# Optimization experiments

Hardware: AMD Instinct MI355X
Metric: run time of the kernel (lower is better)

Reference implementation:

```python
import jax, jax.numpy as jnp
import numpy as np

B, H, W, C = 32, 56, 56, 256
WS = 7            # window size (hard-coded 49=7*7 in original topk modules)
NH = 8            # num heads
HD = C // NH      # head dim = 32
KCH = HD // 2     # channel top-k = 16
KSPT = 28         # spatial top-k
N = WS * WS       # 49 tokens per window
SCALE = HD ** -0.5
MLP_H = 4 * C

def _rel_index(ws):
    coords = np.stack(np.meshgrid(np.arange(ws), np.arange(ws), indexing='ij')).reshape(2, -1)
    rc = (coords[:, :, None] - coords[:, None, :]).transpose(1, 2, 0).astype(np.int64)
    rc[:, :, 0] += ws - 1
    rc[:, :, 1] += ws - 1
    rc[:, :, 0] *= 2 * ws - 1
    return jnp.asarray(rc.sum(-1))  # (N, N)

REL_IDX = _rel_index(WS)

def setup_inputs():
    key = jax.random.key(0)
    ks = jax.random.split(key, 10)
    p = lambda k, shp: jax.random.normal(k, shp, jnp.float32) * 0.02
    return dict(
        x=jax.random.normal(ks[0], (B, H * W, C), jnp.float32),
        norm1_g=jnp.ones((C,), jnp.float32), norm1_b=jnp.zeros((C,), jnp.float32),
        wq=p(ks[1], (C, C)), bq=jnp.zeros((C,), jnp.float32),
        wk=p(ks[2], (C // 2, C // 2)), bk=jnp.zeros((C // 2,), jnp.float32),
        wv=p(ks[3], (C, C)), bv=jnp.zeros((C,), jnp.float32),
        wproj=p(ks[4], (C, C)), bproj=jnp.zeros((C,), jnp.float32),
        wch=p(ks[5], (2 * HD, HD)), bch=jnp.zeros((HD,), jnp.float32),
        rpb_table=p(ks[6], ((2 * WS - 1) ** 2, NH)),
        norm2_g=jnp.ones((C,), jnp.float32), norm2_b=jnp.zeros((C,), jnp.float32),
        w1=p(ks[7], (C, MLP_H)), b1=jnp.zeros((MLP_H,), jnp.float32),
        w2=p(ks[8], (MLP_H, C)), b2=jnp.zeros((C,), jnp.float32),
    )

def _ln(x, g, b):
    mu = x.mean(-1, keepdims=True)
    var = x.var(-1, keepdims=True)
    return (x - mu) / jnp.sqrt(var + 1e-5) * g + b

def reference(x, norm1_g, norm1_b, wq, bq, wk, bk, wv, bv, wproj, bproj,
              wch, bch, rpb_table, norm2_g, norm2_b, w1, b1, w2, b2):
    shortcut = x
    xn = _ln(x, norm1_g, norm1_b).reshape(B, H, W, C)
    # window partition -> (Bw, N, C)
    xw = xn.reshape(B, H // WS, WS, W // WS, WS, C).transpose(0, 1, 3, 2, 4, 5).reshape(-1, N, C)
    Bw = xw.shape[0]
    q = xw @ wq + bq                                                    # (Bw, N, C)
    qh = q.reshape(Bw, N, NH, HD).transpose(0, 2, 1, 3).reshape(Bw * NH, N, HD)
    # ---- channel top-k (ChannelTopk) ----
    feat = jnp.concatenate([qh.mean(1), qh.max(1)], axis=-1)            # (Bn, 2*HD)
    score = jax.nn.softmax(jax.nn.gelu(feat @ wch + bch, approximate=False), axis=1)
    _, cidx = jax.lax.top_k(score, KCH)
    cidx = jnp.sort(cidx, axis=-1)                                      # sorted channel indices
    qcha = jnp.take_along_axis(qh, cidx[:, None, :], axis=2)            # (Bn, N, KCH)
    qcha1 = qcha.reshape(Bw, NH, N, KCH).transpose(0, 2, 1, 3).reshape(Bw, N, C // 2)
    k = qcha1 @ wk + bk                                                 # (Bw, N, C/2)
    # ---- relative position bias ----
    rpb = rpb_table[REL_IDX.reshape(-1)].reshape(N, N, NH).transpose(2, 0, 1)  # (NH, N, N)
    # ---- spatial top-k (SptialTopk) ----
    _, sidx = jax.lax.top_k(qh.mean(-1), KSPT)
    sidx = jnp.sort(sidx, axis=-1)                                      # (Bn, KSPT)
    qal = jnp.take_along_axis(qcha, sidx[:, :, None], axis=1)           # (Bn, KSPT, KCH)
    vsel = jnp.take_along_axis(qh, sidx[:, :, None], axis=1)            # (Bn, KSPT, HD)
    sidx_h = sidx.reshape(Bw, NH, KSPT)
    yal = jnp.take_along_axis(
        jnp.broadcast_to(rpb[None], (Bw, NH, N, N)),
        jnp.broadcast_to(sidx_h[:, :, None, :], (Bw, NH, N, KSPT)), axis=-1)  # (Bw, NH, N, KSPT)
    # ---- attention ----
    v = vsel.reshape(Bw, NH, KSPT, HD).transpose(0, 2, 1, 3).reshape(Bw, KSPT, C)
    v = (v @ wv + bv).reshape(Bw, KSPT, NH, HD).transpose(0, 2, 1, 3)   # (Bw, NH, KSPT, HD)
    qspt = (qal * SCALE).reshape(Bw, NH, KSPT, KCH)
    kh = k.reshape(Bw, N, NH, KCH).transpose(0, 2, 1, 3)                # (Bw, NH, N, KCH)
    attn = jnp.einsum('bnqc,bnkc->bnqk', kh, qspt) + yal                # (Bw, NH, N, KSPT)
    gate = jax.nn.sigmoid(attn.mean(-1))                                # (Bw, NH, N)
    attn = jax.nn.softmax(attn, axis=-1)
    o = jnp.einsum('bnqk,bnkd->bnqd', attn, v) * gate[..., None]        # (Bw, NH, N, HD)
    o = o.transpose(0, 2, 1, 3).reshape(Bw, N, C)
    o = o @ wproj + bproj
    # window reverse -> (B, L, C)
    xr = o.reshape(B, H // WS, W // WS, WS, WS, C).transpose(0, 1, 3, 2, 4, 5).reshape(B, H * W, C)
    x = shortcut + xr
    h = jax.nn.gelu(_ln(x, norm2_g, norm2_b) @ w1 + b1, approximate=False)
    return x + h @ w2 + b2
```

## Files before the change

kernel.cpp:

```cpp
#include <hip/hip_runtime.h>
#include <hip/hip_bf16.h>
#include <cmath>

#define CC 256
#define WSZ 7
#define WWD_ 56
#define NHD 8
#define HDIM 32
#define KCHN 16
#define KSP 28
#define NTOK 49
#define NWIN 2048
#define NBH 16384
#define LL 3136
#define MTOK 100352
#define MLPH 1024
#define SCALE_Q 0.17677669529663689f

typedef float floatx4 __attribute__((ext_vector_type(4)));
typedef __bf16 bf16x8_t __attribute__((ext_vector_type(8)));

__device__ __forceinline__ float gelu_f(float x) {
    return 0.5f * x * (1.0f + erff(x * 0.7071067811865475f));
}

__global__ __launch_bounds__(64) void ln_stats_k(const float* __restrict__ x,
                                                 float* __restrict__ mu,
                                                 float* __restrict__ rs) {
    int row = blockIdx.x;
    int lane = threadIdx.x;
    float4 v = reinterpret_cast<const float4*>(x + (size_t)row * CC)[lane];
    float s = v.x + v.y + v.z + v.w;
    float s2 = v.x * v.x + v.y * v.y + v.z * v.z + v.w * v.w;
#pragma unroll
    for (int off = 32; off > 0; off >>= 1) {
        s += __shfl_down(s, off);
        s2 += __shfl_down(s2, off);
    }
    if (lane == 0) {
        float m = s * (1.0f / CC);
        float var = s2 * (1.0f / CC) - m * m;
        mu[row] = m;
        rs[row] = rsqrtf(var + 1e-5f);
    }
}

struct GP {
    const float* W;
    const float* bias;
    float* C;
    int N, K;
    const float* x;
    const float* mu;
    const float* rs;
    const float* g;
    const float* be;
};

__global__ __launch_bounds__(256) void gemm_q_k(GP p) {
    constexpr int BM = 64, BN = 64, BK = 16;
    __shared__ float As[BK][BM + 4];
    __shared__ float Bs[BK][BN + 4];
    const int bm = blockIdx.x * BM;
    const int bn = blockIdx.y * BN;
    const int tid = threadIdx.x;
    const int tx = tid & 15;
    const int ty = tid >> 4;
    const int rowA = tid >> 2;
    const int ka4 = (tid & 3) << 2;
    const int rowB = tid >> 4;
    const int nb4 = (tid & 15) << 2;
    float acc[4][4] = {};

    const int r = bm + rowA;
    int bwi = r / NTOK, n = r - bwi * NTOK;
    int b = bwi >> 6, rem = bwi & 63;
    int hw = rem >> 3, ww = rem & 7;
    int i0 = n / WSZ, j0 = n - i0 * WSZ;
    size_t grow = (size_t)b * LL + (size_t)(hw * WSZ + i0) * WWD_ + (ww * WSZ + j0);

    for (int k0 = 0; k0 < p.K; k0 += BK) {
        {
            const int kk = k0 + ka4;
            float m = p.mu[grow], rsg = p.rs[grow];
            float4 xv = *reinterpret_cast<const float4*>(p.x + grow * CC + kk);
            float4 gv = *reinterpret_cast<const float4*>(p.g + kk);
            float4 bv = *reinterpret_cast<const float4*>(p.be + kk);
            As[ka4 + 0][rowA] = (xv.x - m) * rsg * gv.x + bv.x;
            As[ka4 + 1][rowA] = (xv.y - m) * rsg * gv.y + bv.y;
            As[ka4 + 2][rowA] = (xv.z - m) * rsg * gv.z + bv.z;
            As[ka4 + 3][rowA] = (xv.w - m) * rsg * gv.w + bv.w;
        }
        {
            float4 bv = *reinterpret_cast<const float4*>(p.W + (size_t)(k0 + rowB) * p.N + bn + nb4);
            Bs[rowB][nb4 + 0] = bv.x;
            Bs[rowB][nb4 + 1] = bv.y;
            Bs[rowB][nb4 + 2] = bv.z;
            Bs[rowB][nb4 + 3] = bv.w;
        }
        __syncthreads();
#pragma unroll
        for (int kk = 0; kk < BK; ++kk) {
            float a[4], bb[4];
#pragma unroll
            for (int u = 0; u < 4; ++u) {
                a[u] = As[kk][ty * 4 + u];
                bb[u] = Bs[kk][tx * 4 + u];
            }
#pragma unroll
            for (int i = 0; i < 4; ++i)
#pragma unroll
                for (int j = 0; j < 4; ++j) acc[i][j] = fmaf(a[i], bb[j], acc[i][j]);
        }
        __syncthreads();
    }
#pragma unroll
    for (int i = 0; i < 4; ++i) {
        const int rr = bm + ty * 4 + i;
#pragma unroll
        for (int j = 0; j < 4; ++j) {
            const int nn = bn + tx * 4 + j;
            p.C[(size_t)rr * p.N + nn] = acc[i][j] + p.bias[nn];
        }
    }
}

struct MG {
    const __hip_bfloat16* A;
    const __hip_bfloat16* B;
    const float* bias;
    int N, K;
    float* Cf;
    __hip_bfloat16* Cb;
    const float* resid;
    int row0;
};

template <int EPI>
__global__ __launch_bounds__(256) void mgemm_k(MG p) {
    __shared__ __align__(16) __hip_bfloat16 As[128 * 32];
    __shared__ __align__(16) __hip_bfloat16 Bs[128 * 32];
    const int bm = blockIdx.x * 128;
    const int bn = blockIdx.y * 128;
    const int t = threadIdx.x;
    const int lane = t & 63;
    const int w = t >> 6;
    const int wm = (w & 1) * 64;
    const int wn = (w >> 1) * 64;
    const int fr = lane & 15;
    const int fk = (lane >> 4) * 8;

    const int m0 = t >> 2, m1 = (t + 256) >> 2;
    const int kc = (t & 3) * 8;
    const __hip_bfloat16* a0 = p.A + (size_t)(bm + m0) * p.K + kc;
    const __hip_bfloat16* a1 = p.A + (size_t)(bm + m1) * p.K + kc;
    const __hip_bfloat16* b0 = p.B + (size_t)(bn + m0) * p.K + kc;
    const __hip_bfloat16* b1 = p.B + (size_t)(bn + m1) * p.K + kc;

    floatx4 acc[4][4] = {};

    for (int k0 = 0; k0 < p.K; k0 += 32) {
        *(uint4*)&As[m0 * 32 + kc] = *(const uint4*)(a0 + k0);
        *(uint4*)&As[m1 * 32 + kc] = *(const uint4*)(a1 + k0);
        *(uint4*)&Bs[m0 * 32 + kc] = *(const uint4*)(b0 + k0);
        *(uint4*)&Bs[m1 * 32 + kc] = *(const uint4*)(b1 + k0);
        __syncthreads();
        bf16x8_t af[4], bf[4];
#pragma unroll
        for (int i = 0; i < 4; ++i)
            af[i] = *(const bf16x8_t*)&As[(wm + i * 16 + fr) * 32 + fk];
#pragma unroll
        for (int j = 0; j < 4; ++j)
            bf[j] = *(const bf16x8_t*)&Bs[(wn + j * 16 + fr) * 32 + fk];
#pragma unroll
        for (int i = 0; i < 4; ++i)
#pragma unroll
            for (int j = 0; j < 4; ++j)
                acc[i][j] = __builtin_amdgcn_mfma_f32_16x16x32_bf16(af[i], bf[j], acc[i][j], 0, 0, 0);
        __syncthreads();
    }

    float bj[4];
#pragma unroll
    for (int j = 0; j < 4; ++j) bj[j] = p.bias[bn + wn + j * 16 + fr];
#pragma unroll
    for (int i = 0; i < 4; ++i) {
#pragma unroll
        for (int r = 0; r < 4; ++r) {
            const int m = bm + wm + i * 16 + (lane >> 4) * 4 + r;
#pragma unroll
            for (int j = 0; j < 4; ++j) {
                const int n = bn + wn + j * 16 + fr;
                float v = acc[i][j][r] + bj[j];
                if constexpr (EPI == 0) {
                    p.Cb[(size_t)m * p.N + n] = __float2bfloat16(v);
                } else if constexpr (EPI == 1) {
                    int bwi = m / NTOK, nn = m - bwi * NTOK;
                    int b = bwi >> 6, rem = bwi & 63;
                    int hw = rem >> 3, wwp = rem & 7;
                    int ii = nn / WSZ, jj = nn - ii * WSZ;
                    size_t oidx = ((size_t)b * LL + (size_t)(hw * WSZ + ii) * WWD_ + (wwp * WSZ + jj)) * CC + n;
                    p.Cf[oidx] = v + p.resid[oidx];
                } else if constexpr (EPI == 2) {
                    p.Cb[(size_t)m * p.N + n] = __float2bfloat16(gelu_f(v));
                } else {
                    size_t gr = (size_t)(m + p.row0);
                    p.Cf[gr * p.N + n] = v + p.resid[gr * p.N + n];
                }
            }
        }
    }
}

__global__ __launch_bounds__(256) void wt_k(const float* __restrict__ W,
                                            __hip_bfloat16* __restrict__ Wt, int K, int N) {
    int g = blockIdx.x * 256 + threadIdx.x;
    if (g >= K * N) return;
    int n = g / K, kk = g - n * K;
    Wt[g] = __float2bfloat16(W[(size_t)kk * N + n]);
}

__global__ __launch_bounds__(64) void topk_k(const float* __restrict__ q,
                                             const float* __restrict__ wch,
                                             const float* __restrict__ bch,
                                             short* __restrict__ cidx,
                                             short* __restrict__ sidx) {
    int bnh = blockIdx.x;
    int bwi = bnh >> 3, h = bnh & 7;
    int lane = threadIdx.x;
    __shared__ float tile[NTOK][HDIM + 1];
    __shared__ float feat[2 * HDIM];
    __shared__ float score[HDIM];
    __shared__ float rowm[NTOK];
    const float* qbase = q + ((size_t)bwi * NTOK) * CC + h * HDIM;
    for (int idx = lane; idx < NTOK * HDIM; idx += 64) {
        int n = idx >> 5, d = idx & 31;
        tile[n][d] = qbase[(size_t)n * CC + d];
    }
    __syncthreads();
    if (lane < HDIM) {
        float s = 0.f, mx = -INFINITY;
        for (int n = 0; n < NTOK; ++n) {
            float v = tile[n][lane];
            s += v;
            mx = fmaxf(mx, v);
        }
        feat[lane] = s * (1.0f / NTOK);
        feat[HDIM + lane] = mx;
    }
    if (lane < NTOK) {
        float s = 0.f;
        for (int d = 0; d < HDIM; ++d) s += tile[lane][d];
        rowm[lane] = s;
    }
    __syncthreads();
    if (lane < HDIM) {
        float s = bch[lane];
        for (int j = 0; j < 2 * HDIM; ++j) s += feat[j] * wch[j * HDIM + lane];
        score[lane] = gelu_f(s);
    }
    __syncthreads();
    {
        bool sel = false;
        if (lane < HDIM) {
            float sv = score[lane];
            int rank = 0;
            for (int j = 0; j < HDIM; ++j) {
                float oj = score[j];
                rank += (oj > sv) || (oj == sv && j < lane);
            }
            sel = rank < KCHN;
        }
        unsigned long long m = __ballot(sel);
        if (sel) {
            int pos = __popcll(m & ((1ull << lane) - 1ull));
            cidx[(size_t)bnh * KCHN + pos] = (short)lane;
        }
    }
    {
        bool sel = false;
        if (lane < NTOK) {
            float sv = rowm[lane];
            int rank = 0;
            for (int j = 0; j < NTOK; ++j) {
                float oj = rowm[j];
                rank += (oj > sv) || (oj == sv && j < lane);
            }
            sel = rank < KSP;
        }
        unsigned long long m = __ballot(sel);
        if (sel) {
            int pos = __popcll(m & ((1ull << lane) - 1ull));
            sidx[(size_t)bnh * KSP + pos] = (short)lane;
        }
    }
}

__global__ __launch_bounds__(256) void gather_ch_k(const float* __restrict__ q,
                                                   const short* __restrict__ cidx,
                                                   __hip_bfloat16* __restrict__ ak) {
    int g = blockIdx.x * 256 + threadIdx.x;
    int r = g >> 7, kk = g & 127;
    int bwi = r / NTOK;
    int hp = kk >> 4, c = kk & 15;
    int ci = cidx[((size_t)(bwi * NHD + hp)) * KCHN + c];
    ak[g] = __float2bfloat16(q[(size_t)r * CC + hp * HDIM + ci]);
}

__global__ __launch_bounds__(256) void gather_sp_k(const float* __restrict__ q,
                                                   const short* __restrict__ sidx,
                                                   __hip_bfloat16* __restrict__ av) {
    int g = blockIdx.x * 256 + threadIdx.x;
    int rr = g >> 8, c = g & 255;
    int bwi = rr / KSP, s = rr - bwi * KSP;
    int tok = sidx[((size_t)(bwi * NHD + (c >> 5))) * KSP + s];
    av[g] = __float2bfloat16(q[((size_t)(bwi * NTOK + tok)) * CC + c]);
}

__global__ __launch_bounds__(64) void attn_k(const float* __restrict__ q,
                                             const __hip_bfloat16* __restrict__ kb,
                                             const __hip_bfloat16* __restrict__ vb,
                                             const short* __restrict__ cidx,
                                             const short* __restrict__ sidx,
                                             const float* __restrict__ rpb,
                                             __hip_bfloat16* __restrict__ ob) {
    int bnh = blockIdx.x;
    int bwi = bnh >> 3, h = bnh & 7;
    int lane = threadIdx.x;
    __shared__ float kh_s[NTOK][KCHN + 1];
    __shared__ float qs_s[KSP][KCHN];
    __shared__ float v_s[KSP][HDIM];
    __shared__ int sidx_s[KSP];
    __shared__ int cidx_s[KCHN];
    if (lane < KSP) sidx_s[lane] = sidx[(size_t)bnh * KSP + lane];
    if (lane < KCHN) cidx_s[lane] = cidx[(size_t)bnh * KCHN + lane];
    for (int idx = lane; idx < NTOK * KCHN; idx += 64) {
        int n = idx >> 4, c = idx & 15;
        kh_s[n][c] = __bfloat162float(kb[((size_t)bwi * NTOK + n) * (NHD * KCHN) + h * KCHN + c]);
    }
    for (int idx = lane; idx < KSP * HDIM; idx += 64) {
        int s = idx >> 5, d = idx & 31;
        v_s[s][d] = __bfloat162float(vb[((size_t)bwi * KSP + s) * CC + h * HDIM + d]);
    }
    __syncthreads();
    for (int idx = lane; idx < KSP * KCHN; idx += 64) {
        int s = idx >> 4, c = idx & 15;
        qs_s[s][c] = q[((size_t)bwi * NTOK + sidx_s[s]) * CC + h * HDIM + cidx_s[c]] * SCALE_Q;
    }
    __syncthreads();
    if (lane < NTOK) {
        int i1 = lane / WSZ, j1 = lane - i1 * WSZ;
        float a[KSP];
        float msum = 0.f;
#pragma unroll
        for (int s = 0; s < KSP; ++s) {
            float dot = 0.f;
#pragma unroll
            for (int c = 0; c < KCHN; ++c) dot += kh_s[lane][c] * qs_s[s][c];
            int m = sidx_s[s];
            int i2 = m / WSZ, j2 = m - i2 * WSZ;
            float bias = rpb[(size_t)((i1 - i2 + 6) * 13 + (j1 - j2 + 6)) * NHD + h];
            a[s] = dot + bias;
            msum += a[s];
        }
        float gate = 1.0f / (1.0f + expf(-msum * (1.0f / KSP)));
        float mx = -INFINITY;
#pragma unroll
        for (int s = 0; s < KSP; ++s) mx = fmaxf(mx, a[s]);
        float sum = 0.f;
#pragma unroll
        for (int s = 0; s < KSP; ++s) {
            a[s] = expf(a[s] - mx);
            sum += a[s];
        }
        float inv = gate / sum;
        __hip_bfloat16* orow = ob + ((size_t)bwi * NTOK + lane) * CC + h * HDIM;
#pragma unroll
        for (int d = 0; d < HDIM; ++d) {
            float od = 0.f;
#pragma unroll
            for (int s = 0; s < KSP; ++s) od += a[s] * v_s[s][d];
            orow[d] = __float2bfloat16(od * inv);
        }
    }
}

__global__ __launch_bounds__(64) void ln2_k(const float* __restrict__ x2,
                                            const float* __restrict__ g,
                                            const float* __restrict__ b,
                                            __hip_bfloat16* __restrict__ a2) {
    int row = blockIdx.x;
    int lane = threadIdx.x;
    float4 v = reinterpret_cast<const float4*>(x2 + (size_t)row * CC)[lane];
    float s = v.x + v.y + v.z + v.w;
    float s2 = v.x * v.x + v.y * v.y + v.z * v.z + v.w * v.w;
#pragma unroll
    for (int off = 1; off < 64; off <<= 1) {
        s += __shfl_xor(s, off);
        s2 += __shfl_xor(s2, off);
    }
    float m = s * (1.0f / CC);
    float rsg = rsqrtf(s2 * (1.0f / CC) - m * m + 1e-5f);
    float4 gv = reinterpret_cast<const float4*>(g)[lane];
    float4 bv = reinterpret_cast<const float4*>(b)[lane];
    __hip_bfloat16* orow = a2 + (size_t)row * CC + lane * 4;
    orow[0] = __float2bfloat16((v.x - m) * rsg * gv.x + bv.x);
    orow[1] = __float2bfloat16((v.y - m) * rsg * gv.y + bv.y);
    orow[2] = __float2bfloat16((v.z - m) * rsg * gv.z + bv.z);
    orow[3] = __float2bfloat16((v.w - m) * rsg * gv.w + bv.w);
}

extern "C" void kernel_launch(void* const* d_in, const int* in_sizes, int n_in,
                              void* d_out, int out_size, void* d_ws, size_t ws_size,
                              hipStream_t stream) {
    const float* x   = (const float*)d_in[0];
    const float* n1g = (const float*)d_in[1];
    const float* n1b = (const float*)d_in[2];
    const float* wq  = (const float*)d_in[3];
    const float* bq  = (const float*)d_in[4];
    const float* wk  = (const float*)d_in[5];
    const float* bk  = (const float*)d_in[6];
    const float* wv  = (const float*)d_in[7];
    const float* bv  = (const float*)d_in[8];
    const float* wpj = (const float*)d_in[9];
    const float* bpj = (const float*)d_in[10];
    const float* wch = (const float*)d_in[11];
    const float* bch = (const float*)d_in[12];
    const float* rpb = (const float*)d_in[13];
    const float* n2g = (const float*)d_in[14];
    const float* n2b = (const float*)d_in[15];
    const float* w1  = (const float*)d_in[16];
    const float* b1  = (const float*)d_in[17];
    const float* w2  = (const float*)d_in[18];
    const float* b2  = (const float*)d_in[19];
    float* out = (float*)d_out;

    char* wsb = (char*)d_ws;
    float* qb            = (float*)wsb;
    __hip_bfloat16* g1   = (__hip_bfloat16*)(wsb + 102760448);
    __hip_bfloat16* g2   = (__hip_bfloat16*)(wsb + 128450560);
    __hip_bfloat16* ob   = g1;
    __hip_bfloat16* kb   = (__hip_bfloat16*)(wsb + 157810688);
    __hip_bfloat16* vb   = (__hip_bfloat16*)(wsb + 183500800);
    float* mu1           = (float*)(wsb + 212860928);
    float* rs1           = mu1 + MTOK;
    short* cidx          = (short*)(wsb + 213663744);
    short* sidx          = (short*)(wsb + 214188032);
    __hip_bfloat16* wkt  = (__hip_bfloat16*)(wsb + 215105536);
    __hip_bfloat16* wvt  = (__hip_bfloat16*)(wsb + 215138304);
    __hip_bfloat16* wpt  = (__hip_bfloat16*)(wsb + 215269376);
    __hip_bfloat16* w1t  = (__hip_bfloat16*)(wsb + 215400448);
    __hip_bfloat16* w2t  = (__hip_bfloat16*)(wsb + 215924736);
    __hip_bfloat16* a2   = (__hip_bfloat16*)qb;
    __hip_bfloat16* hb   = (__hip_bfloat16*)(wsb + 51380224);
    if (ws_size < 216449024ULL) return;

    wt_k<<<(128 * 128 + 255) / 256, 256, 0, stream>>>(wk, wkt, 128, 128);
    wt_k<<<(256 * 256 + 255) / 256, 256, 0, stream>>>(wv, wvt, 256, 256);
    wt_k<<<(256 * 256 + 255) / 256, 256, 0, stream>>>(wpj, wpt, 256, 256);
    wt_k<<<(256 * 1024 + 255) / 256, 256, 0, stream>>>(w1, w1t, 256, 1024);
    wt_k<<<(1024 * 256 + 255) / 256, 256, 0, stream>>>(w2, w2t, 1024, 256);

    ln_stats_k<<<MTOK, 64, 0, stream>>>(x, mu1, rs1);

    GP p{};
    p.W = wq; p.bias = bq; p.C = qb; p.N = CC; p.K = CC;
    p.x = x; p.mu = mu1; p.rs = rs1; p.g = n1g; p.be = n1b;
    gemm_q_k<<<dim3(MTOK / 64, CC / 64), 256, 0, stream>>>(p);

    topk_k<<<NBH, 64, 0, stream>>>(qb, wch, bch, cidx, sidx);

    gather_ch_k<<<MTOK * 128 / 256, 256, 0, stream>>>(qb, cidx, g1);
    MG m{};
    m.A = g1; m.B = wkt; m.bias = bk; m.N = 128; m.K = 128; m.Cb = kb;
    mgemm_k<0><<<dim3(MTOK / 128, 1), 256, 0, stream>>>(m);

    gather_sp_k<<<NWIN * KSP * 256 / 256, 256, 0, stream>>>(qb, sidx, g2);
    m = MG{};
    m.A = g2; m.B = wvt; m.bias = bv; m.N = CC; m.K = CC; m.Cb = vb;
    mgemm_k<0><<<dim3(NWIN * KSP / 128, 2), 256, 0, stream>>>(m);

    attn_k<<<NBH, 64, 0, stream>>>(qb, kb, vb, cidx, sidx, rpb, ob);

    m = MG{};
    m.A = ob; m.B = wpt; m.bias = bpj; m.N = CC; m.K = CC; m.Cf = out; m.resid = x;
    mgemm_k<1><<<dim3(MTOK / 128, 2), 256, 0, stream>>>(m);

    ln2_k<<<MTOK, 64, 0, stream>>>(out, n2g, n2b, a2);

    const int CHUNK = MTOK / 4;
    for (int c = 0; c < 4; ++c) {
        int start = c * CHUNK;
        m = MG{};
        m.A = a2 + (size_t)start * CC; m.B = w1t; m.bias = b1;
        m.N = MLPH; m.K = CC; m.Cb = hb;
        mgemm_k<2><<<dim3(CHUNK / 128, MLPH / 128), 256, 0, stream>>>(m);

        m = MG{};
        m.A = hb; m.B = w2t; m.bias = b2; m.N = CC; m.K = MLPH;
        m.Cf = out; m.resid = out; m.row0 = start;
        mgemm_k<3><<<dim3(CHUNK / 128, CC / 128), 256, 0, stream>>>(m);
    }
}
```

Before: 1.147 ms.

## Widen Q GEMM tile to full N and load tiles via direct global-to-LDS DMA

After: 1.141 ms. Within noise of the previous version (-0.6%).

```diff
diff --git a/kernel.cpp b/kernel.cpp
--- a/kernel.cpp
+++ b/kernel.cpp
@@ -24,6 +24,11 @@
     return 0.5f * x * (1.0f + erff(x * 0.7071067811865475f));
 }
 
+__device__ __forceinline__ void lds_dma16(const void* g, void* l) {
+    __builtin_amdgcn_global_load_lds((__attribute__((address_space(1))) void*)(void*)g,
+                                     (__attribute__((address_space(3))) void*)l, 16, 0, 0);
+}
+
 __global__ __launch_bounds__(64) void ln_stats_k(const float* __restrict__ x,
                                                  float* __restrict__ mu,
                                                  float* __restrict__ rs) {
@@ -58,70 +63,70 @@
 };
 
 __global__ __launch_bounds__(256) void gemm_q_k(GP p) {
-    constexpr int BM = 64, BN = 64, BK = 16;
-    __shared__ float As[BK][BM + 4];
-    __shared__ float Bs[BK][BN + 4];
-    const int bm = blockIdx.x * BM;
-    const int bn = blockIdx.y * BN;
-    const int tid = threadIdx.x;
-    const int tx = tid & 15;
-    const int ty = tid >> 4;
-    const int rowA = tid >> 2;
-    const int ka4 = (tid & 3) << 2;
-    const int rowB = tid >> 4;
-    const int nb4 = (tid & 15) << 2;
-    float acc[4][4] = {};
-
-    const int r = bm + rowA;
+    __shared__ __align__(16) float As[16][68];
+    __shared__ __align__(16) float Bs[16][256];
+    const int bm = blockIdx.x * 64;
+    const int t = threadIdx.x;
+    const int tx = t & 31;
+    const int ty = t >> 5;
+    const int w = t >> 6;
+
+    const int ar = t >> 2;
+    const int ak = (t & 3) * 4;
+
+    const int r = bm + ar;
     int bwi = r / NTOK, n = r - bwi * NTOK;
     int b = bwi >> 6, rem = bwi & 63;
     int hw = rem >> 3, ww = rem & 7;
     int i0 = n / WSZ, j0 = n - i0 * WSZ;
     size_t grow = (size_t)b * LL + (size_t)(hw * WSZ + i0) * WWD_ + (ww * WSZ + j0);
-
-    for (int k0 = 0; k0 < p.K; k0 += BK) {
+    const float m = p.mu[grow], rsg = p.rs[grow];
+    const float* xrow = p.x + grow * CC;
+
+    float acc[8][8] = {};
+
+    for (int k0 = 0; k0 < CC; k0 += 16) {
         {
-            const int kk = k0 + ka4;
-            float m = p.mu[grow], rsg = p.rs[grow];
-            float4 xv = *reinterpret_cast<const float4*>(p.x + grow * CC + kk);
+            const int kk = k0 + ak;
+            float4 xv = *reinterpret_cast<const float4*>(xrow + kk);
             float4 gv = *reinterpret_cast<const float4*>(p.g + kk);
             float4 bv = *reinterpret_cast<const float4*>(p.be + kk);
-            As[ka4 + 0][rowA] = (xv.x - m) * rsg * gv.x + bv.x;
-            As[ka4 + 1][rowA] = (xv.y - m) * rsg * gv.y + bv.y;
-            As[ka4 + 2][rowA] = (xv.z - m) * rsg * gv.z + bv.z;
-            As[ka4 + 3][rowA] = (xv.w - m) * rsg * gv.w + bv.w;
-        }
-        {
-            float4 bv = *reinterpret_cast<const float4*>(p.W + (size_t)(k0 + rowB) * p.N + bn + nb4);
-            Bs[rowB][nb4 + 0] = bv.x;
-            Bs[rowB][nb4 + 1] = bv.y;
-            Bs[rowB][nb4 + 2] = bv.z;
-            Bs[rowB][nb4 + 3] = bv.w;
+            As[ak + 0][ar] = (xv.x - m) * rsg * gv.x + bv.x;
+            As[ak + 1][ar] = (xv.y - m) * rsg * gv.y + bv.y;
+            As[ak + 2][ar] = (xv.z - m) * rsg * gv.z + bv.z;
+            As[ak + 3][ar] = (xv.w - m) * rsg * gv.w + bv.w;
+        }
+#pragma unroll
+        for (int j = 0; j < 4; ++j) {
+            const int c = j * 256 + t;
+            const float* gp = p.W + (size_t)(k0 + (c >> 6)) * CC + (c & 63) * 4;
+            lds_dma16(gp, (char*)&Bs[0][0] + j * 4096 + w * 1024);
         }
         __syncthreads();
 #pragma unroll
-        for (int kk = 0; kk < BK; ++kk) {
-            float a[4], bb[4];
-#pragma unroll
-            for (int u = 0; u < 4; ++u) {
-                a[u] = As[kk][ty * 4 + u];
-                bb[u] = Bs[kk][tx * 4 + u];
-            }
-#pragma unroll
-            for (int i = 0; i < 4; ++i)
-#pragma unroll
-                for (int j = 0; j < 4; ++j) acc[i][j] = fmaf(a[i], bb[j], acc[i][j]);
+        for (int kk = 0; kk < 16; ++kk) {
+            float a[8], bb[8];
+            *(float4*)&a[0] = *(const float4*)&As[kk][ty * 8];
+            *(float4*)&a[4] = *(const float4*)&As[kk][ty * 8 + 4];
+            *(float4*)&bb[0] = *(const float4*)&Bs[kk][tx * 8];
+            *(float4*)&bb[4] = *(const float4*)&Bs[kk][tx * 8 + 4];
+#pragma unroll
+            for (int i = 0; i < 8; ++i)
+#pragma unroll
+                for (int j = 0; j < 8; ++j) acc[i][j] = fmaf(a[i], bb[j], acc[i][j]);
         }
         __syncthreads();
     }
-#pragma unroll
-    for (int i = 0; i < 4; ++i) {
-        const int rr = bm + ty * 4 + i;
-#pragma unroll
-        for (int j = 0; j < 4; ++j) {
-            const int nn = bn + tx * 4 + j;
-            p.C[(size_t)rr * p.N + nn] = acc[i][j] + p.bias[nn];
-        }
+
+    float bj[8];
+#pragma unroll
+    for (int j = 0; j < 8; ++j) bj[j] = p.bias[tx * 8 + j];
+#pragma unroll
+    for (int i = 0; i < 8; ++i) {
+        const int row = bm + ty * 8 + i;
+        float* crow = p.C + (size_t)row * CC + tx * 8;
+#pragma unroll
+        for (int j = 0; j < 8; ++j) crow[j] = acc[i][j] + bj[j];
     }
 }
 
@@ -160,10 +165,10 @@
     floatx4 acc[4][4] = {};
 
     for (int k0 = 0; k0 < p.K; k0 += 32) {
-        *(uint4*)&As[m0 * 32 + kc] = *(const uint4*)(a0 + k0);
-        *(uint4*)&As[m1 * 32 + kc] = *(const uint4*)(a1 + k0);
-        *(uint4*)&Bs[m0 * 32 + kc] = *(const uint4*)(b0 + k0);
-        *(uint4*)&Bs[m1 * 32 + kc] = *(const uint4*)(b1 + k0);
+        lds_dma16(a0 + k0, &As[w * 512]);
+        lds_dma16(a1 + k0, &As[2048 + w * 512]);
+        lds_dma16(b0 + k0, &Bs[w * 512]);
+        lds_dma16(b1 + k0, &Bs[2048 + w * 512]);
         __syncthreads();
         bf16x8_t af[4], bf[4];
 #pragma unroll
@@ -466,7 +471,7 @@
     GP p{};
     p.W = wq; p.bias = bq; p.C = qb; p.N = CC; p.K = CC;
     p.x = x; p.mu = mu1; p.rs = rs1; p.g = n1g; p.be = n1b;
-    gemm_q_k<<<dim3(MTOK / 64, CC / 64), 256, 0, stream>>>(p);
+    gemm_q_k<<<dim3(MTOK / 64), 256, 0, stream>>>(p);
 
     topk_k<<<NBH, 64, 0, stream>>>(qb, wch, bch, cidx, sidx);
 
```
